# Kernel tuning notes

Measured on AMD Instinct MI355X. Metric: run time of the kernel, lower is better.

The kernel has to match this reference:

```python
import jax, jax.numpy as jnp
import numpy as np

N = 100000

def gcn_conv(x, edge_index, W, b):
    # PyG GCNConv: h = x @ W; add self-loops; norm = deg^-1/2[src]*deg^-1/2[dst]; scatter-add; + b
    n = x.shape[0]
    loops = jnp.arange(n, dtype=edge_index.dtype)
    src = jnp.concatenate([edge_index[0], loops])
    dst = jnp.concatenate([edge_index[1], loops])
    deg = jax.ops.segment_sum(jnp.ones_like(dst, dtype=x.dtype), dst, num_segments=n)
    dinv = jnp.where(deg > 0, jax.lax.rsqrt(deg), 0.0)
    norm = dinv[src] * dinv[dst]              # [E+n]
    h = x @ W                                  # [n, out]
    msg = h[src] * norm[:, None]               # [E+n, out] gather
    out = jax.ops.segment_sum(msg, dst, num_segments=n)  # scatter-add
    return out + b


def setup_inputs() -> dict:
    key = jax.random.key(0)
    k1, k2, k3, k4, k5, k6 = jax.random.split(key, 6)
    x = jax.random.normal(k1, (N, 100), dtype=jnp.float32)
    edge_index = jax.random.randint(k2, (2, 1600000), 0, N, dtype=jnp.int64)
    W1 = jax.random.normal(k3, (100, 128), dtype=jnp.float32) * (1.0 / np.sqrt(100))
    b1 = jnp.zeros((128,), dtype=jnp.float32)
    W2 = jax.random.normal(k4, (128, 64), dtype=jnp.float32) * (1.0 / np.sqrt(128))
    b2 = jnp.zeros((64,), dtype=jnp.float32)
    return {"x": x, "W1": W1, "b1": b1, "W2": W2, "b2": b2, "edge_index": edge_index}


def reference(x, W1, b1, W2, b2, edge_index):
    h = gcn_conv(x, edge_index, W1, b1)
    h = jax.nn.relu(h)
    out = gcn_conv(h, edge_index, W2, b2)
    return out
```

## Files before the change

kernel.cpp:

```cpp
#include <hip/hip_runtime.h>

#define NN 100000
#define F_IN 100
#define F1 128
#define F2 64
#define CAP 64
#define FP 8
#define FS 256


__device__ __forceinline__ unsigned short f2bf(float f) {
    unsigned int u = __float_as_uint(f);
    u = (u + 0x7FFFu + ((u >> 16) & 1u)) >> 16;
    return (unsigned short)u;
}
__device__ __forceinline__ float bflo(unsigned int v) { return __uint_as_float(v << 16); }
__device__ __forceinline__ float bfhi(unsigned int v) { return __uint_as_float(v & 0xFFFF0000u); }
__device__ __forceinline__ unsigned int pack2(float lo, float hi) {
    return (unsigned int)f2bf(lo) | ((unsigned int)f2bf(hi) << 16);
}


__global__ __launch_bounds__(256) void fill_part_kernel(const int* __restrict__ ei,
                                                        int* __restrict__ cur,
                                                        int* __restrict__ adj,
                                                        int E, int n, int npp) {
    const int p = blockIdx.x & (FP - 1);
    const int s = blockIdx.x >> 3;
    const int lo = p * npp;
    const int hi = min(n, lo + npp);
    const int per = (E + FS - 1) / FS;
    const int e0 = s * per;
    const int e1 = min(E, e0 + per);
    for (int e = e0 + threadIdx.x; e < e1; e += 256) {
        const int d = ei[E + e];
        if (d >= lo && d < hi) {
            const int src = ei[e];
            const int pos = atomicAdd(&cur[d], 1);
            if (pos < CAP) adj[(size_t)d * CAP + pos] = src;
        }
    }
}

__global__ __launch_bounds__(256) void dinv_kernel(const int* __restrict__ deg,
                                                   float* __restrict__ dinv, int n) {
    int i = blockIdx.x * blockDim.x + threadIdx.x;
    if (i < n) dinv[i] = rsqrtf((float)(deg[i] + 1));
}


__global__ __launch_bounds__(256) void gemm1_kernel(const float* __restrict__ x,
                                                    const float* __restrict__ W,
                                                    const float* __restrict__ dinv,
                                                    unsigned short* __restrict__ g, int n) {
    __shared__ float Ws[F_IN * F1];
    __shared__ float xs[F_IN * 64];
    const int tid = threadIdx.x;
    const int row0 = blockIdx.x * 64;

    for (int i = tid; i < F_IN * F1 / 4; i += 256)
        *(float4*)&Ws[i * 4] = *(const float4*)&W[i * 4];

    for (int i = tid; i < 25 * 64; i += 256) {
        const int c4 = i >> 6;
        const int r  = i & 63;
        const int row = row0 + r;
        float4 v = make_float4(0.f, 0.f, 0.f, 0.f);
        if (row < n) v = *(const float4*)&x[(size_t)row * F_IN + c4 * 4];
        xs[(c4 * 4 + 0) * 64 + r] = v.x;
        xs[(c4 * 4 + 1) * 64 + r] = v.y;
        xs[(c4 * 4 + 2) * 64 + r] = v.z;
        xs[(c4 * 4 + 3) * 64 + r] = v.w;
    }
    __syncthreads();

    const int c0 = (tid & 15) * 4;
    const int r0 = (tid >> 4) * 4;

    float acc[4][8];
#pragma unroll
    for (int i = 0; i < 4; ++i)
#pragma unroll
        for (int j = 0; j < 8; ++j) acc[i][j] = 0.f;

#pragma unroll 2
    for (int k = 0; k < F_IN; ++k) {
        const float4 xv = *(const float4*)&xs[k * 64 + r0];
        const float4 w0 = *(const float4*)&Ws[k * F1 + c0];
        const float4 w1 = *(const float4*)&Ws[k * F1 + c0 + 64];
        const float xr[4] = {xv.x, xv.y, xv.z, xv.w};
#pragma unroll
        for (int i = 0; i < 4; ++i) {
            acc[i][0] += xr[i] * w0.x; acc[i][1] += xr[i] * w0.y;
            acc[i][2] += xr[i] * w0.z; acc[i][3] += xr[i] * w0.w;
            acc[i][4] += xr[i] * w1.x; acc[i][5] += xr[i] * w1.y;
            acc[i][6] += xr[i] * w1.z; acc[i][7] += xr[i] * w1.w;
        }
    }

#pragma unroll
    for (int i = 0; i < 4; ++i) {
        const int row = row0 + r0 + i;
        if (row >= n) break;
        const float dv = dinv[row];
        ushort4 oa, ob;
        oa.x = f2bf(acc[i][0] * dv); oa.y = f2bf(acc[i][1] * dv);
        oa.z = f2bf(acc[i][2] * dv); oa.w = f2bf(acc[i][3] * dv);
        ob.x = f2bf(acc[i][4] * dv); ob.y = f2bf(acc[i][5] * dv);
        ob.z = f2bf(acc[i][6] * dv); ob.w = f2bf(acc[i][7] * dv);
        *(ushort4*)&g[(size_t)row * F1 + c0]      = oa;
        *(ushort4*)&g[(size_t)row * F1 + c0 + 64] = ob;
    }
}


__global__ __launch_bounds__(256) void gemm2_kernel(const unsigned short* __restrict__ h,
                                                    const float* __restrict__ W,
                                                    const float* __restrict__ dinv,
                                                    unsigned short* __restrict__ g, int n) {
    __shared__ float Ws[F1 * F2];
    __shared__ float xs[F1 * 64];
    const int tid = threadIdx.x;
    const int row0 = blockIdx.x * 64;

    for (int i = tid; i < F1 * F2 / 4; i += 256)
        *(float4*)&Ws[i * 4] = *(const float4*)&W[i * 4];

    for (int i = tid; i < 16 * 64; i += 256) {
        const int c8 = (i >> 6) * 8;
        const int r  = i & 63;
        const int row = row0 + r;
        uint4 v = make_uint4(0u, 0u, 0u, 0u);
        if (row < n) v = *(const uint4*)&h[(size_t)row * F1 + c8];
        xs[(c8 + 0) * 64 + r] = bflo(v.x);
        xs[(c8 + 1) * 64 + r] = bfhi(v.x);
        xs[(c8 + 2) * 64 + r] = bflo(v.y);
        xs[(c8 + 3) * 64 + r] = bfhi(v.y);
        xs[(c8 + 4) * 64 + r] = bflo(v.z);
        xs[(c8 + 5) * 64 + r] = bfhi(v.z);
        xs[(c8 + 6) * 64 + r] = bflo(v.w);
        xs[(c8 + 7) * 64 + r] = bfhi(v.w);
    }
    __syncthreads();

    const int c0 = (tid & 15) * 4;
    const int r0 = (tid >> 4) * 4;

    float acc[4][4];
#pragma unroll
    for (int i = 0; i < 4; ++i)
#pragma unroll
        for (int j = 0; j < 4; ++j) acc[i][j] = 0.f;

#pragma unroll 2
    for (int k = 0; k < F1; ++k) {
        const float4 xv = *(const float4*)&xs[k * 64 + r0];
        const float4 w  = *(const float4*)&Ws[k * F2 + c0];
        const float xr[4] = {xv.x, xv.y, xv.z, xv.w};
#pragma unroll
        for (int i = 0; i < 4; ++i) {
            acc[i][0] += xr[i] * w.x; acc[i][1] += xr[i] * w.y;
            acc[i][2] += xr[i] * w.z; acc[i][3] += xr[i] * w.w;
        }
    }

#pragma unroll
    for (int i = 0; i < 4; ++i) {
        const int row = row0 + r0 + i;
        if (row >= n) break;
        const float dv = dinv[row];
        ushort4 o;
        o.x = f2bf(acc[i][0] * dv); o.y = f2bf(acc[i][1] * dv);
        o.z = f2bf(acc[i][2] * dv); o.w = f2bf(acc[i][3] * dv);
        *(ushort4*)&g[(size_t)row * F2 + c0] = o;
    }
}


__global__ __launch_bounds__(256) void gather128_relu_kernel(const uint4* __restrict__ g,
                                                             const int* __restrict__ adj,
                                                             const int* __restrict__ deg,
                                                             const float* __restrict__ dinv,
                                                             const float* __restrict__ b,
                                                             uint4* __restrict__ out, int n) {
    const int node = (int)((blockIdx.x * (size_t)blockDim.x + threadIdx.x) >> 6);
    if (node >= n) return;
    const int lane = threadIdx.x & 63;
    const int c = lane & 15;
    const int q = lane >> 4;
    const size_t base = (size_t)node * CAP;
    const int nd = min(deg[node], CAP);

    float a0 = 0.f, a1 = 0.f, a2 = 0.f, a3 = 0.f;
    float a4 = 0.f, a5 = 0.f, a6 = 0.f, a7 = 0.f;
    if (q == 0) {
        const uint4 sv = g[(size_t)node * 16 + c];
        a0 = bflo(sv.x); a1 = bfhi(sv.x); a2 = bflo(sv.y); a3 = bfhi(sv.y);
        a4 = bflo(sv.z); a5 = bfhi(sv.z); a6 = bflo(sv.w); a7 = bfhi(sv.w);
    }

    const int av = (lane < nd) ? adj[base + lane] : 0;
    const int iters = (nd + 3) >> 2;
    for (int i = 0; i < iters; ++i) {
        const int t = 4 * i + q;
        const int s = __shfl(av, (t < nd) ? t : 0);
        const uint4 v = g[(size_t)s * 16 + c];
        if (t < nd) {
            a0 += bflo(v.x); a1 += bfhi(v.x);
            a2 += bflo(v.y); a3 += bfhi(v.y);
            a4 += bflo(v.z); a5 += bfhi(v.z);
            a6 += bflo(v.w); a7 += bfhi(v.w);
        }
    }

    a0 += __shfl_xor(a0, 16); a1 += __shfl_xor(a1, 16);
    a2 += __shfl_xor(a2, 16); a3 += __shfl_xor(a3, 16);
    a4 += __shfl_xor(a4, 16); a5 += __shfl_xor(a5, 16);
    a6 += __shfl_xor(a6, 16); a7 += __shfl_xor(a7, 16);
    a0 += __shfl_xor(a0, 32); a1 += __shfl_xor(a1, 32);
    a2 += __shfl_xor(a2, 32); a3 += __shfl_xor(a3, 32);
    a4 += __shfl_xor(a4, 32); a5 += __shfl_xor(a5, 32);
    a6 += __shfl_xor(a6, 32); a7 += __shfl_xor(a7, 32);

    if (q == 0) {
        const float dv = dinv[node];
        const float4 b0 = *(const float4*)&b[c * 8];
        const float4 b1 = *(const float4*)&b[c * 8 + 4];
        uint4 o;
        o.x = pack2(fmaxf(dv * a0 + b0.x, 0.f), fmaxf(dv * a1 + b0.y, 0.f));
        o.y = pack2(fmaxf(dv * a2 + b0.z, 0.f), fmaxf(dv * a3 + b0.w, 0.f));
        o.z = pack2(fmaxf(dv * a4 + b1.x, 0.f), fmaxf(dv * a5 + b1.y, 0.f));
        o.w = pack2(fmaxf(dv * a6 + b1.z, 0.f), fmaxf(dv * a7 + b1.w, 0.f));
        out[(size_t)node * 16 + c] = o;
    }
}


__global__ __launch_bounds__(256) void gather64_kernel(const uint4* __restrict__ g,
                                                       const int* __restrict__ adj,
                                                       const int* __restrict__ deg,
                                                       const float* __restrict__ dinv,
                                                       const float* __restrict__ b,
                                                       float* __restrict__ out, int n) {
    const int node = (int)((blockIdx.x * (size_t)blockDim.x + threadIdx.x) >> 6);
    if (node >= n) return;
    const int lane = threadIdx.x & 63;
    const int c  = lane & 7;
    const int o8 = lane >> 3;
    const size_t base = (size_t)node * CAP;
    const int nd = min(deg[node], CAP);

    float a0 = 0.f, a1 = 0.f, a2 = 0.f, a3 = 0.f;
    float a4 = 0.f, a5 = 0.f, a6 = 0.f, a7 = 0.f;
    if (o8 == 0) {
        const uint4 sv = g[(size_t)node * 8 + c];
        a0 = bflo(sv.x); a1 = bfhi(sv.x); a2 = bflo(sv.y); a3 = bfhi(sv.y);
        a4 = bflo(sv.z); a5 = bfhi(sv.z); a6 = bflo(sv.w); a7 = bfhi(sv.w);
    }

    const int av = (lane < nd) ? adj[base + lane] : 0;
    const int iters = (nd + 7) >> 3;
    for (int i = 0; i < iters; ++i) {
        const int t = 8 * i + o8;
        const int s = __shfl(av, (t < nd) ? t : 0);
        const uint4 v = g[(size_t)s * 8 + c];
        if (t < nd) {
            a0 += bflo(v.x); a1 += bfhi(v.x);
            a2 += bflo(v.y); a3 += bfhi(v.y);
            a4 += bflo(v.z); a5 += bfhi(v.z);
            a6 += bflo(v.w); a7 += bfhi(v.w);
        }
    }

#pragma unroll
    for (int d = 8; d <= 32; d <<= 1) {
        a0 += __shfl_xor(a0, d); a1 += __shfl_xor(a1, d);
        a2 += __shfl_xor(a2, d); a3 += __shfl_xor(a3, d);
        a4 += __shfl_xor(a4, d); a5 += __shfl_xor(a5, d);
        a6 += __shfl_xor(a6, d); a7 += __shfl_xor(a7, d);
    }

    if (o8 == 0) {
        const float dv = dinv[node];
        const float4 b0 = *(const float4*)&b[c * 8];
        const float4 b1 = *(const float4*)&b[c * 8 + 4];
        float4 u, w;
        u.x = dv * a0 + b0.x; u.y = dv * a1 + b0.y;
        u.z = dv * a2 + b0.z; u.w = dv * a3 + b0.w;
        w.x = dv * a4 + b1.x; w.y = dv * a5 + b1.y;
        w.z = dv * a6 + b1.z; w.w = dv * a7 + b1.w;
        *(float4*)&out[(size_t)node * F2 + c * 8]     = u;
        *(float4*)&out[(size_t)node * F2 + c * 8 + 4] = w;
    }
}


extern "C" void kernel_launch(void* const* d_in, const int* in_sizes, int n_in,
                              void* d_out, int out_size, void* d_ws, size_t ws_size,
                              hipStream_t stream) {
    const float* x  = (const float*)d_in[0];
    const float* W1 = (const float*)d_in[1];
    const float* b1 = (const float*)d_in[2];
    const float* W2 = (const float*)d_in[3];
    const float* b2 = (const float*)d_in[4];
    const int*   ei = (const int*)d_in[5];

    const int n = in_sizes[0] / F_IN;
    const int E = in_sizes[5] / 2;
    float* out = (float*)d_out;

    char* ws = (char*)d_ws;
    int*   cur  = (int*)(ws);
    float* dinv = (float*)(ws + 524288);
    int*   adj  = (int*)(ws + 1048576);
    unsigned short* g1 = (unsigned short*)(ws + 29360128);
    unsigned short* h2 = (unsigned short*)(ws + 58720256);
    unsigned short* g2 = (unsigned short*)(ws + 88080384);

    hipMemsetAsync(cur, 0, (size_t)n * 4, stream);

    {
        const int npp = (n + FP - 1) / FP;
        fill_part_kernel<<<FS * FP, 256, 0, stream>>>(ei, cur, adj, E, n, npp);
    }
    dinv_kernel<<<(n + 255) / 256, 256, 0, stream>>>(cur, dinv, n);

    gemm1_kernel<<<(n + 63) / 64, 256, 0, stream>>>(x, W1, dinv, g1, n);
    gather128_relu_kernel<<<(n * 64 + 255) / 256, 256, 0, stream>>>(
        (const uint4*)g1, adj, cur, dinv, b1, (uint4*)h2, n);

    gemm2_kernel<<<(n + 63) / 64, 256, 0, stream>>>(h2, W2, dinv, g2, n);
    gather64_kernel<<<(n * 64 + 255) / 256, 256, 0, stream>>>(
        (const uint4*)g2, adj, cur, dinv, b2, out, n);
}
```

Before: 357.4 us.

## Enlarge GEMM tiles to 128 rows, pack operands as bf16 pairs, inline dinv

Both GEMM kernels now process 128 rows per block with 8x8 (gemm1) or 8x4 (gemm2) register tiles per thread. W1 and the gemm2 input are held in shared memory as packed bf16 pairs, which halves their LDS footprint and the load count per k-step. The separate dinv kernel and its buffer are removed, and each kernel computes rsqrt(deg+1) inline. W1 is now rounded to bf16, which lowers precision, and the larger tiles raise register and LDS pressure, which may cut occupancy.

Result: slower. 382.4 us (+7.0%).

```diff
diff --git a/kernel.cpp b/kernel.cpp
--- a/kernel.cpp
+++ b/kernel.cpp
@@ -42,137 +42,138 @@
     }
 }
 
-__global__ __launch_bounds__(256) void dinv_kernel(const int* __restrict__ deg,
-                                                   float* __restrict__ dinv, int n) {
-    int i = blockIdx.x * blockDim.x + threadIdx.x;
-    if (i < n) dinv[i] = rsqrtf((float)(deg[i] + 1));
-}
-
 
 __global__ __launch_bounds__(256) void gemm1_kernel(const float* __restrict__ x,
                                                     const float* __restrict__ W,
-                                                    const float* __restrict__ dinv,
+                                                    const int* __restrict__ deg,
                                                     unsigned short* __restrict__ g, int n) {
-    __shared__ float Ws[F_IN * F1];
-    __shared__ float xs[F_IN * 64];
+    __shared__ unsigned int Ws2[50][F1];
+    __shared__ float xs[F_IN][128];
     const int tid = threadIdx.x;
-    const int row0 = blockIdx.x * 64;
-
-    for (int i = tid; i < F_IN * F1 / 4; i += 256)
-        *(float4*)&Ws[i * 4] = *(const float4*)&W[i * 4];
-
-    for (int i = tid; i < 25 * 64; i += 256) {
-        const int c4 = i >> 6;
-        const int r  = i & 63;
+    const int row0 = blockIdx.x * 128;
+
+    for (int i = tid; i < 50 * F1; i += 256) {
+        const int kk = i >> 7, c = i & 127;
+        Ws2[kk][c] = pack2(W[(2 * kk) * F1 + c], W[(2 * kk + 1) * F1 + c]);
+    }
+    for (int i = tid; i < 25 * 128; i += 256) {
+        const int c4 = i >> 7;
+        const int r  = i & 127;
         const int row = row0 + r;
         float4 v = make_float4(0.f, 0.f, 0.f, 0.f);
         if (row < n) v = *(const float4*)&x[(size_t)row * F_IN + c4 * 4];
-        xs[(c4 * 4 + 0) * 64 + r] = v.x;
-        xs[(c4 * 4 + 1) * 64 + r] = v.y;
-        xs[(c4 * 4 + 2) * 64 + r] = v.z;
-        xs[(c4 * 4 + 3) * 64 + r] = v.w;
+        xs[c4 * 4 + 0][r] = v.x;
+        xs[c4 * 4 + 1][r] = v.y;
+        xs[c4 * 4 + 2][r] = v.z;
+        xs[c4 * 4 + 3][r] = v.w;
     }
     __syncthreads();
 
-    const int c0 = (tid & 15) * 4;
-    const int r0 = (tid >> 4) * 4;
-
-    float acc[4][8];
-#pragma unroll
-    for (int i = 0; i < 4; ++i)
+    const int c0 = (tid & 15) * 8;
+    const int r0 = (tid >> 4) * 8;
+
+    float acc[8][8];
+#pragma unroll
+    for (int i = 0; i < 8; ++i)
 #pragma unroll
         for (int j = 0; j < 8; ++j) acc[i][j] = 0.f;
 
-#pragma unroll 2
-    for (int k = 0; k < F_IN; ++k) {
-        const float4 xv = *(const float4*)&xs[k * 64 + r0];
-        const float4 w0 = *(const float4*)&Ws[k * F1 + c0];
-        const float4 w1 = *(const float4*)&Ws[k * F1 + c0 + 64];
-        const float xr[4] = {xv.x, xv.y, xv.z, xv.w};
-#pragma unroll
-        for (int i = 0; i < 4; ++i) {
-            acc[i][0] += xr[i] * w0.x; acc[i][1] += xr[i] * w0.y;
-            acc[i][2] += xr[i] * w0.z; acc[i][3] += xr[i] * w0.w;
-            acc[i][4] += xr[i] * w1.x; acc[i][5] += xr[i] * w1.y;
-            acc[i][6] += xr[i] * w1.z; acc[i][7] += xr[i] * w1.w;
-        }
-    }
-
-#pragma unroll
-    for (int i = 0; i < 4; ++i) {
+    for (int kk = 0; kk < 50; ++kk) {
+        const float4 xa = *(const float4*)&xs[2 * kk][r0];
+        const float4 xb = *(const float4*)&xs[2 * kk][r0 + 4];
+        const float4 xc = *(const float4*)&xs[2 * kk + 1][r0];
+        const float4 xd = *(const float4*)&xs[2 * kk + 1][r0 + 4];
+        const uint4 wu = *(const uint4*)&Ws2[kk][c0];
+        const uint4 wv = *(const uint4*)&Ws2[kk][c0 + 4];
+        const float xr0[8] = {xa.x, xa.y, xa.z, xa.w, xb.x, xb.y, xb.z, xb.w};
+        const float xr1[8] = {xc.x, xc.y, xc.z, xc.w, xd.x, xd.y, xd.z, xd.w};
+        const unsigned int wp[8] = {wu.x, wu.y, wu.z, wu.w, wv.x, wv.y, wv.z, wv.w};
+        float w0[8], w1[8];
+#pragma unroll
+        for (int j = 0; j < 8; ++j) { w0[j] = bflo(wp[j]); w1[j] = bfhi(wp[j]); }
+#pragma unroll
+        for (int i = 0; i < 8; ++i)
+#pragma unroll
+            for (int j = 0; j < 8; ++j)
+                acc[i][j] += xr0[i] * w0[j] + xr1[i] * w1[j];
+    }
+
+#pragma unroll
+    for (int i = 0; i < 8; ++i) {
         const int row = row0 + r0 + i;
         if (row >= n) break;
-        const float dv = dinv[row];
-        ushort4 oa, ob;
-        oa.x = f2bf(acc[i][0] * dv); oa.y = f2bf(acc[i][1] * dv);
-        oa.z = f2bf(acc[i][2] * dv); oa.w = f2bf(acc[i][3] * dv);
-        ob.x = f2bf(acc[i][4] * dv); ob.y = f2bf(acc[i][5] * dv);
-        ob.z = f2bf(acc[i][6] * dv); ob.w = f2bf(acc[i][7] * dv);
-        *(ushort4*)&g[(size_t)row * F1 + c0]      = oa;
-        *(ushort4*)&g[(size_t)row * F1 + c0 + 64] = ob;
+        const float dv = rsqrtf((float)(deg[row] + 1));
+        uint4 o;
+        o.x = pack2(acc[i][0] * dv, acc[i][1] * dv);
+        o.y = pack2(acc[i][2] * dv, acc[i][3] * dv);
+        o.z = pack2(acc[i][4] * dv, acc[i][5] * dv);
+        o.w = pack2(acc[i][6] * dv, acc[i][7] * dv);
+        *(uint4*)&g[(size_t)row * F1 + c0] = o;
     }
 }
 
 
 __global__ __launch_bounds__(256) void gemm2_kernel(const unsigned short* __restrict__ h,
                                                     const float* __restrict__ W,
-                                                    const float* __restrict__ dinv,
+                                                    const int* __restrict__ deg,
                                                     unsigned short* __restrict__ g, int n) {
+    __shared__ unsigned int xs2[64][128];
     __shared__ float Ws[F1 * F2];
-    __shared__ float xs[F1 * 64];
     const int tid = threadIdx.x;
-    const int row0 = blockIdx.x * 64;
+    const int row0 = blockIdx.x * 128;
 
     for (int i = tid; i < F1 * F2 / 4; i += 256)
         *(float4*)&Ws[i * 4] = *(const float4*)&W[i * 4];
 
-    for (int i = tid; i < 16 * 64; i += 256) {
-        const int c8 = (i >> 6) * 8;
-        const int r  = i & 63;
+    for (int i = tid; i < 16 * 128; i += 256) {
+        const int c8 = (i >> 7) * 8;
+        const int r  = i & 127;
         const int row = row0 + r;
         uint4 v = make_uint4(0u, 0u, 0u, 0u);
         if (row < n) v = *(const uint4*)&h[(size_t)row * F1 + c8];
-        xs[(c8 + 0) * 64 + r] = bflo(v.x);
-        xs[(c8 + 1) * 64 + r] = bfhi(v.x);
-        xs[(c8 + 2) * 64 + r] = bflo(v.y);
-        xs[(c8 + 3) * 64 + r] = bfhi(v.y);
-        xs[(c8 + 4) * 64 + r] = bflo(v.z);
-        xs[(c8 + 5) * 64 + r] = bfhi(v.z);
-        xs[(c8 + 6) * 64 + r] = bflo(v.w);
-        xs[(c8 + 7) * 64 + r] = bfhi(v.w);
+        xs2[(c8 >> 1) + 0][r] = v.x;
+        xs2[(c8 >> 1) + 1][r] = v.y;
+        xs2[(c8 >> 1) + 2][r] = v.z;
+        xs2[(c8 >> 1) + 3][r] = v.w;
     }
     __syncthreads();
 
     const int c0 = (tid & 15) * 4;
-    const int r0 = (tid >> 4) * 4;
-
-    float acc[4][4];
-#pragma unroll
-    for (int i = 0; i < 4; ++i)
+    const int r0 = (tid >> 4) * 8;
+
+    float acc[8][4];
+#pragma unroll
+    for (int i = 0; i < 8; ++i)
 #pragma unroll
         for (int j = 0; j < 4; ++j) acc[i][j] = 0.f;
 
-#pragma unroll 2
-    for (int k = 0; k < F1; ++k) {
-        const float4 xv = *(const float4*)&xs[k * 64 + r0];
-        const float4 w  = *(const float4*)&Ws[k * F2 + c0];
-        const float xr[4] = {xv.x, xv.y, xv.z, xv.w};
-#pragma unroll
-        for (int i = 0; i < 4; ++i) {
-            acc[i][0] += xr[i] * w.x; acc[i][1] += xr[i] * w.y;
-            acc[i][2] += xr[i] * w.z; acc[i][3] += xr[i] * w.w;
+    for (int kk = 0; kk < 64; ++kk) {
+        const uint4 xp0 = *(const uint4*)&xs2[kk][r0];
+        const uint4 xp1 = *(const uint4*)&xs2[kk][r0 + 4];
+        const float4 wv0 = *(const float4*)&Ws[(2 * kk) * F2 + c0];
+        const float4 wv1 = *(const float4*)&Ws[(2 * kk + 1) * F2 + c0];
+        const unsigned int up[8] = {xp0.x, xp0.y, xp0.z, xp0.w, xp1.x, xp1.y, xp1.z, xp1.w};
+        const float wa[4] = {wv0.x, wv0.y, wv0.z, wv0.w};
+        const float wb[4] = {wv1.x, wv1.y, wv1.z, wv1.w};
+#pragma unroll
+        for (int i = 0; i < 8; ++i) {
+            const float h0 = bflo(up[i]);
+            const float h1 = bfhi(up[i]);
+#pragma unroll
+            for (int j = 0; j < 4; ++j)
+                acc[i][j] += h0 * wa[j] + h1 * wb[j];
         }
     }
 
 #pragma unroll
-    for (int i = 0; i < 4; ++i) {
+    for (int i = 0; i < 8; ++i) {
         const int row = row0 + r0 + i;
         if (row >= n) break;
-        const float dv = dinv[row];
-        ushort4 o;
-        o.x = f2bf(acc[i][0] * dv); o.y = f2bf(acc[i][1] * dv);
-        o.z = f2bf(acc[i][2] * dv); o.w = f2bf(acc[i][3] * dv);
-        *(ushort4*)&g[(size_t)row * F2 + c0] = o;
+        const float dv = rsqrtf((float)(deg[row] + 1));
+        uint2 o;
+        o.x = pack2(acc[i][0] * dv, acc[i][1] * dv);
+        o.y = pack2(acc[i][2] * dv, acc[i][3] * dv);
+        *(uint2*)&g[(size_t)row * F2 + c0] = o;
     }
 }
 
@@ -180,7 +181,6 @@
 __global__ __launch_bounds__(256) void gather128_relu_kernel(const uint4* __restrict__ g,
                                                              const int* __restrict__ adj,
                                                              const int* __restrict__ deg,
-                                                             const float* __restrict__ dinv,
                                                              const float* __restrict__ b,
                                                              uint4* __restrict__ out, int n) {
     const int node = (int)((blockIdx.x * (size_t)blockDim.x + threadIdx.x) >> 6);
@@ -189,7 +189,8 @@
     const int c = lane & 15;
     const int q = lane >> 4;
     const size_t base = (size_t)node * CAP;
-    const int nd = min(deg[node], CAP);
+    const int ndraw = deg[node];
+    const int nd = min(ndraw, CAP);
 
     float a0 = 0.f, a1 = 0.f, a2 = 0.f, a3 = 0.f;
     float a4 = 0.f, a5 = 0.f, a6 = 0.f, a7 = 0.f;
@@ -223,7 +224,7 @@
     a6 += __shfl_xor(a6, 32); a7 += __shfl_xor(a7, 32);
 
     if (q == 0) {
-        const float dv = dinv[node];
+        const float dv = rsqrtf((float)(ndraw + 1));
         const float4 b0 = *(const float4*)&b[c * 8];
         const float4 b1 = *(const float4*)&b[c * 8 + 4];
         uint4 o;
@@ -239,7 +240,6 @@
 __global__ __launch_bounds__(256) void gather64_kernel(const uint4* __restrict__ g,
                                                        const int* __restrict__ adj,
                                                        const int* __restrict__ deg,
-                                                       const float* __restrict__ dinv,
                                                        const float* __restrict__ b,
                                                        float* __restrict__ out, int n) {
     const int node = (int)((blockIdx.x * (size_t)blockDim.x + threadIdx.x) >> 6);
@@ -248,7 +248,8 @@
     const int c  = lane & 7;
     const int o8 = lane >> 3;
     const size_t base = (size_t)node * CAP;
-    const int nd = min(deg[node], CAP);
+    const int ndraw = deg[node];
+    const int nd = min(ndraw, CAP);
 
     float a0 = 0.f, a1 = 0.f, a2 = 0.f, a3 = 0.f;
     float a4 = 0.f, a5 = 0.f, a6 = 0.f, a7 = 0.f;
@@ -281,7 +282,7 @@
     }
 
     if (o8 == 0) {
-        const float dv = dinv[node];
+        const float dv = rsqrtf((float)(ndraw + 1));
         const float4 b0 = *(const float4*)&b[c * 8];
         const float4 b1 = *(const float4*)&b[c * 8 + 4];
         float4 u, w;
@@ -310,9 +311,8 @@
     float* out = (float*)d_out;
 
     char* ws = (char*)d_ws;
-    int*   cur  = (int*)(ws);
-    float* dinv = (float*)(ws + 524288);
-    int*   adj  = (int*)(ws + 1048576);
+    int* cur = (int*)(ws);
+    int* adj = (int*)(ws + 1048576);
     unsigned short* g1 = (unsigned short*)(ws + 29360128);
     unsigned short* h2 = (unsigned short*)(ws + 58720256);
     unsigned short* g2 = (unsigned short*)(ws + 88080384);
@@ -323,13 +323,12 @@
         const int npp = (n + FP - 1) / FP;
         fill_part_kernel<<<FS * FP, 256, 0, stream>>>(ei, cur, adj, E, n, npp);
     }
-    dinv_kernel<<<(n + 255) / 256, 256, 0, stream>>>(cur, dinv, n);
-
-    gemm1_kernel<<<(n + 63) / 64, 256, 0, stream>>>(x, W1, dinv, g1, n);
+
+    gemm1_kernel<<<(n + 127) / 128, 256, 0, stream>>>(x, W1, cur, g1, n);
     gather128_relu_kernel<<<(n * 64 + 255) / 256, 256, 0, stream>>>(
-        (const uint4*)g1, adj, cur, dinv, b1, (uint4*)h2, n);
-
-    gemm2_kernel<<<(n + 63) / 64, 256, 0, stream>>>(h2, W2, dinv, g2, n);
+        (const uint4*)g1, adj, cur, b1, (uint4*)h2, n);
+
+    gemm2_kernel<<<(n + 127) / 128, 256, 0, stream>>>(h2, W2, cur, g2, n);
     gather64_kernel<<<(n * 64 + 255) / 256, 256, 0, stream>>>(
-        (const uint4*)g2, adj, cur, dinv, b2, out, n);
-}
+        (const uint4*)g2, adj, cur, b2, out, n);
+}
```
